# Kernel tuning notes

Hardware: AMD Instinct MI355X
Metric: run time of the kernel (lower is better)

## Reference

```python
import jax, jax.numpy as jnp
import numpy as np

HEADS = 16
EPS = 1e-5

def _ln(x, g, b):
    m = jnp.mean(x, axis=-1, keepdims=True)
    v = jnp.mean((x - m) ** 2, axis=-1, keepdims=True)
    return (x - m) * jax.lax.rsqrt(v + EPS) * g + b

def setup_inputs() -> dict:
    key = jax.random.key(0)
    ks = jax.random.split(key, 12)
    B, N, C, H = 4, 2048, 1024, 4096
    d = {}
    d['x'] = jax.random.normal(ks[0], (B, N, C), jnp.float32)
    d['pos_embed'] = jax.random.normal(ks[1], (1, N, C), jnp.float32)
    # LayerNorm params (normq, normk, normv, norm)
    for nm in ['nq', 'nk', 'nv', 'n']:
        d[nm + '_g'] = jnp.ones((C,), jnp.float32)
        d[nm + '_b'] = jnp.zeros((C,), jnp.float32)
    s = 1.0 / np.sqrt(C)
    d['wq'] = jax.random.uniform(ks[2], (C, C), jnp.float32, -s, s)
    d['bq'] = jnp.zeros((C,), jnp.float32)
    d['wk'] = jax.random.uniform(ks[3], (C, C), jnp.float32, -s, s)
    d['bk'] = jnp.zeros((C,), jnp.float32)
    d['wv'] = jax.random.uniform(ks[4], (C, C), jnp.float32, -s, s)
    d['bv'] = jnp.zeros((C,), jnp.float32)
    d['wp'] = jax.random.uniform(ks[5], (C, C), jnp.float32, -s, s)
    d['bp'] = jnp.zeros((C,), jnp.float32)
    d['w1'] = jax.random.uniform(ks[6], (C, H), jnp.float32, -s, s)
    d['b1'] = jnp.zeros((H,), jnp.float32)
    sh = 1.0 / np.sqrt(H)
    d['w2'] = jax.random.uniform(ks[7], (H, C), jnp.float32, -sh, sh)
    d['b2'] = jnp.zeros((C,), jnp.float32)
    return d

def reference(x, pos_embed, nq_g, nq_b, nk_g, nk_b, nv_g, nv_b, wq, bq, wk, bk, wv, bv, wp, bp, n_g, n_b, w1, b1, w2, b2):
    B, N, C = x.shape
    hd = C // HEADS
    scale = hd ** -0.5
    q_in = x
    k_in = x + pos_embed
    v_in = x + pos_embed
    # Attention (eval mode: dropout = identity)
    q = (_ln(q_in, nq_g, nq_b) @ wq + bq).reshape(B, N, HEADS, hd)
    k = (_ln(k_in, nk_g, nk_b) @ wk + bk).reshape(B, N, HEADS, hd)
    v = (_ln(v_in, nv_g, nv_b) @ wv + bv).reshape(B, N, HEADS, hd)
    attn = jnp.einsum('bqhd,bkhd->bhqk', q, k) * scale
    attn = jax.nn.softmax(attn, axis=-1)
    out = jnp.einsum('bhqk,bkhd->bqhd', attn, v).reshape(B, N, C)
    out = out @ wp + bp
    # residual + MLP
    h = q_in + out
    y = _ln(h, n_g, n_b) @ w1 + b1
    y = jnp.where(y >= 0, y, 0.1 * y)  # LeakyReLU(0.1)
    y = y @ w2 + b2
    return h + y
```

## Files before the change

kernel.cpp:

```cpp
#include <hip/hip_runtime.h>
#include <hip/hip_bf16.h>

#define DEV __device__ __forceinline__

typedef __attribute__((ext_vector_type(8))) short short8;
typedef __attribute__((ext_vector_type(4))) float f32x4;
typedef __attribute__((ext_vector_type(4))) int i32x4;

constexpr int Bb   = 4;
constexpr int SEQ  = 2048;
constexpr int C    = 1024;
constexpr int HID  = 4096;
constexpr int NH   = 16;
constexpr int HD   = 64;
constexpr int MTOT = Bb * SEQ;

DEV unsigned bfbits(float f) {
  unsigned x = __float_as_uint(f);
  return (x + 0x7fffu + ((x >> 16) & 1u)) >> 16;
}

DEV short f2bf(float f) { return (short)bfbits(f); }

DEV unsigned packbf(float a, float b) {
  return bfbits(a) | (bfbits(b) << 16);
}

DEV void gload16(const void* g, void* l) {
  __builtin_amdgcn_global_load_lds((const __attribute__((address_space(1))) void*)g,
                                   (__attribute__((address_space(3))) void*)l, 16, 0, 0);
}

__global__ void k_transpose_w(const float* __restrict__ src, short* __restrict__ dst,
                              int R, int Cc) {
  __shared__ float t[32][33];
  int tx = threadIdx.x & 31, ty = threadIdx.x >> 5;
  int c0 = blockIdx.x * 32, r0 = blockIdx.y * 32;
  #pragma unroll
  for (int i = 0; i < 4; i++)
    t[ty + i * 8][tx] = src[(size_t)(r0 + ty + i * 8) * Cc + c0 + tx];
  __syncthreads();
  #pragma unroll
  for (int i = 0; i < 4; i++)
    dst[(size_t)(c0 + ty + i * 8) * R + r0 + tx] = f2bf(t[tx][ty + i * 8]);
}

__global__ void k_transpose_v(const short* __restrict__ V, short* __restrict__ Vt) {
  __shared__ short t[32][33];
  int tx = threadIdx.x & 31, ty = threadIdx.x >> 5;
  int plane = blockIdx.z;
  int b = plane >> 4, h = plane & 15;
  int n0 = blockIdx.x * 32, d0 = blockIdx.y * 32;
  #pragma unroll
  for (int i = 0; i < 4; i++)
    t[ty + i * 8][tx] = V[(size_t)(b * SEQ + n0 + ty + i * 8) * C + h * HD + d0 + tx];
  __syncthreads();
  #pragma unroll
  for (int i = 0; i < 4; i++)
    Vt[((size_t)plane * HD + d0 + ty + i * 8) * SEQ + n0 + tx] = t[tx][ty + i * 8];
}

__global__ void k_ln_qkv(const float* __restrict__ x, const float* __restrict__ pos,
                         const float* __restrict__ nqg, const float* __restrict__ nqb,
                         const float* __restrict__ nkg, const float* __restrict__ nkb,
                         const float* __restrict__ nvg, const float* __restrict__ nvb,
                         short* __restrict__ xq, short* __restrict__ xk,
                         short* __restrict__ xv) {
  int row = blockIdx.x, tid = threadIdx.x;
  int n = row & (SEQ - 1);
  float a4[4], p4[4];
  float s1 = 0, s2 = 0, t1 = 0, t2 = 0;
  #pragma unroll
  for (int i = 0; i < 4; i++) {
    int c = tid + i * 256;
    float a = x[(size_t)row * C + c];
    float p = pos[(size_t)n * C + c] + a;
    a4[i] = a; p4[i] = p;
    s1 += a; s2 += a * a; t1 += p; t2 += p * p;
  }
  #pragma unroll
  for (int off = 32; off; off >>= 1) {
    s1 += __shfl_xor(s1, off, 64);
    s2 += __shfl_xor(s2, off, 64);
    t1 += __shfl_xor(t1, off, 64);
    t2 += __shfl_xor(t2, off, 64);
  }
  __shared__ float red[4][4];
  int wave = tid >> 6, lane = tid & 63;
  if (lane == 0) { red[wave][0] = s1; red[wave][1] = s2; red[wave][2] = t1; red[wave][3] = t2; }
  __syncthreads();
  s1 = red[0][0] + red[1][0] + red[2][0] + red[3][0];
  s2 = red[0][1] + red[1][1] + red[2][1] + red[3][1];
  t1 = red[0][2] + red[1][2] + red[2][2] + red[3][2];
  t2 = red[0][3] + red[1][3] + red[2][3] + red[3][3];
  float mq = s1 * (1.f / C), mk = t1 * (1.f / C);
  float rq = rsqrtf(s2 * (1.f / C) - mq * mq + 1e-5f);
  float rk = rsqrtf(t2 * (1.f / C) - mk * mk + 1e-5f);
  #pragma unroll
  for (int i = 0; i < 4; i++) {
    int c = tid + i * 256;
    float nq_ = (a4[i] - mq) * rq;
    float nk_ = (p4[i] - mk) * rk;
    xq[(size_t)row * C + c] = f2bf(nq_ * nqg[c] + nqb[c]);
    xk[(size_t)row * C + c] = f2bf(nk_ * nkg[c] + nkb[c]);
    xv[(size_t)row * C + c] = f2bf(nk_ * nvg[c] + nvb[c]);
  }
}

__global__ void k_ln1(const float* __restrict__ h, const float* __restrict__ g,
                      const float* __restrict__ bta, short* __restrict__ out) {
  int row = blockIdx.x, tid = threadIdx.x;
  float a4[4];
  float s1 = 0, s2 = 0;
  #pragma unroll
  for (int i = 0; i < 4; i++) {
    int c = tid + i * 256;
    float a = h[(size_t)row * C + c];
    a4[i] = a; s1 += a; s2 += a * a;
  }
  #pragma unroll
  for (int off = 32; off; off >>= 1) {
    s1 += __shfl_xor(s1, off, 64);
    s2 += __shfl_xor(s2, off, 64);
  }
  __shared__ float red[4][2];
  int wave = tid >> 6, lane = tid & 63;
  if (lane == 0) { red[wave][0] = s1; red[wave][1] = s2; }
  __syncthreads();
  s1 = red[0][0] + red[1][0] + red[2][0] + red[3][0];
  s2 = red[0][1] + red[1][1] + red[2][1] + red[3][1];
  float m = s1 * (1.f / C);
  float r = rsqrtf(s2 * (1.f / C) - m * m + 1e-5f);
  #pragma unroll
  for (int i = 0; i < 4; i++) {
    int c = tid + i * 256;
    out[(size_t)row * C + c] = f2bf((a4[i] - m) * r * g[c] + bta[c]);
  }
}

template <int MODE>
__global__ __launch_bounds__(256, 2)
void k_gemm(const short* __restrict__ A, const short* __restrict__ Bt,
            const float* __restrict__ bias, const float* __restrict__ resid,
            void* __restrict__ outp, int Nn, int Kk) {
  __shared__ short sA[128 * 32];
  __shared__ short sB[128 * 32];
  const int tid = threadIdx.x;
  const int n0 = blockIdx.x * 128, m0 = blockIdx.y * 128;
  const int wave = tid >> 6, lane = tid & 63, quad = lane >> 4, l15 = lane & 15;
  const int wm = (wave >> 1) * 64, wn = (wave & 1) * 64;

  const int r0 = tid >> 2, s0 = (tid & 3) * 8;
  const short* gA0 = A + (size_t)(m0 + r0) * Kk + s0;
  const short* gA1 = A + (size_t)(m0 + r0 + 64) * Kk + s0;
  const short* gB0 = Bt + (size_t)(n0 + r0) * Kk + s0;
  const short* gB1 = Bt + (size_t)(n0 + r0 + 64) * Kk + s0;
  short* lA0 = &sA[tid * 8];
  short* lA1 = &sA[(tid + 256) * 8];
  short* lB0 = &sB[tid * 8];
  short* lB1 = &sB[(tid + 256) * 8];

  const f32x4 fzero = {0.f, 0.f, 0.f, 0.f};
  f32x4 acc[4][4];
  #pragma unroll
  for (int mi = 0; mi < 4; mi++)
    #pragma unroll
    for (int ni = 0; ni < 4; ni++) acc[mi][ni] = fzero;

  for (int k0 = 0; k0 < Kk; k0 += 32) {
    gload16(gA0 + k0, lA0);
    gload16(gA1 + k0, lA1);
    gload16(gB0 + k0, lB0);
    gload16(gB1 + k0, lB1);
    __syncthreads();
    short8 av[4], bv[4];
    #pragma unroll
    for (int mi = 0; mi < 4; mi++)
      av[mi] = *(const short8*)&sA[(wm + mi * 16 + l15) * 32 + quad * 8];
    #pragma unroll
    for (int ni = 0; ni < 4; ni++)
      bv[ni] = *(const short8*)&sB[(wn + ni * 16 + l15) * 32 + quad * 8];
    #pragma unroll
    for (int mi = 0; mi < 4; mi++)
      #pragma unroll
      for (int ni = 0; ni < 4; ni++)
        acc[mi][ni] = __builtin_amdgcn_mfma_f32_16x16x32_bf16(av[mi], bv[ni], acc[mi][ni], 0, 0, 0);
    __syncthreads();
  }

  float bb[4];
  #pragma unroll
  for (int ni = 0; ni < 4; ni++) bb[ni] = bias[n0 + wn + ni * 16 + l15];

  #pragma unroll
  for (int mi = 0; mi < 4; mi++) {
    #pragma unroll
    for (int ni = 0; ni < 4; ni++) {
      #pragma unroll
      for (int r = 0; r < 4; r++) {
        int row = m0 + wm + mi * 16 + quad * 4 + r;
        int col = n0 + wn + ni * 16 + l15;
        float v = acc[mi][ni][r] + bb[ni];
        if constexpr (MODE == 1) v = v >= 0.f ? v : 0.1f * v;
        if constexpr (MODE == 3) v *= 0.125f;
        if constexpr (MODE == 2)
          ((float*)outp)[(size_t)row * Nn + col] = resid[(size_t)row * Nn + col] + v;
        else
          ((short*)outp)[(size_t)row * Nn + col] = f2bf(v);
      }
    }
  }
}

__global__ __launch_bounds__(256, 4)
void k_attn(const short* __restrict__ Q, const short* __restrict__ K,
            const short* __restrict__ Vt, short* __restrict__ O) {
  constexpr int LD = 72;
  __shared__ short sQ[128 * LD];
  __shared__ short sK[64 * LD];
  __shared__ short sV[64 * LD];
  const int tid = threadIdx.x;
  const int bh = blockIdx.y;
  const int b = bh >> 4, h = bh & 15;
  const int q0 = blockIdx.x * 128;
  const int wave = tid >> 6, lane = tid & 63, quad = lane >> 4, l15 = lane & 15;
  const int wm = wave * 32;
  const size_t tokBase = (size_t)b * SEQ;

  #pragma unroll
  for (int i = 0; i < 4; i++) {
    int idx = tid + i * 256, row = idx >> 3, seg = idx & 7;
    *(int4*)&sQ[row * LD + seg * 8] =
        *(const int4*)(Q + (tokBase + q0 + row) * C + h * HD + seg * 8);
  }

  const f32x4 fzero = {0.f, 0.f, 0.f, 0.f};
  f32x4 o[2][4];
  float lsum[2] = {0.f, 0.f};
  #pragma unroll
  for (int qi = 0; qi < 2; qi++)
    #pragma unroll
    for (int di = 0; di < 4; di++) o[qi][di] = fzero;

  const int selHi = quad >> 1;
  const int srcL0 = ((quad & 1) * 2) * 16 + l15;
  const int srcL1 = ((quad & 1) * 2 + 1) * 16 + l15;

  for (int kb = 0; kb < SEQ / 64; kb++) {
    const int k0 = kb * 64;
    __syncthreads();
    #pragma unroll
    for (int i = 0; i < 2; i++) {
      int idx = tid + i * 256, row = idx >> 3, seg = idx & 7;
      *(int4*)&sK[row * LD + seg * 8] =
          *(const int4*)(K + (tokBase + k0 + row) * C + h * HD + seg * 8);
      *(int4*)&sV[row * LD + seg * 8] =
          *(const int4*)(Vt + ((size_t)bh * HD + row) * SEQ + k0 + seg * 8);
    }
    __syncthreads();

    unsigned pk[4][2][2];
    float csum[2] = {0.f, 0.f};
    #pragma unroll
    for (int qi = 0; qi < 2; qi++) {
      short8 b0 = *(const short8*)&sQ[(wm + qi * 16 + l15) * LD + quad * 8];
      short8 b1 = *(const short8*)&sQ[(wm + qi * 16 + l15) * LD + 32 + quad * 8];
      #pragma unroll
      for (int ki = 0; ki < 4; ki++) {
        short8 a0 = *(const short8*)&sK[(ki * 16 + l15) * LD + quad * 8];
        short8 a1 = *(const short8*)&sK[(ki * 16 + l15) * LD + 32 + quad * 8];
        f32x4 st = __builtin_amdgcn_mfma_f32_16x16x32_bf16(a0, b0, fzero, 0, 0, 0);
        st = __builtin_amdgcn_mfma_f32_16x16x32_bf16(a1, b1, st, 0, 0, 0);
        float p0 = __expf(st[0]), p1 = __expf(st[1]);
        float p2 = __expf(st[2]), p3 = __expf(st[3]);
        csum[qi] += (p0 + p1) + (p2 + p3);
        pk[ki][qi][0] = packbf(p0, p1);
        pk[ki][qi][1] = packbf(p2, p3);
      }
    }
    #pragma unroll
    for (int qi = 0; qi < 2; qi++) {
      float v = csum[qi];
      v += __shfl_xor(v, 16, 64);
      v += __shfl_xor(v, 32, 64);
      lsum[qi] += v;
    }

    #pragma unroll
    for (int kc = 0; kc < 2; kc++) {
      #pragma unroll
      for (int qi = 0; qi < 2; qi++) {
        i32x4 fr;
        int vA, vB;
        vA = __shfl((int)pk[2 * kc][qi][0], srcL0, 64);
        vB = __shfl((int)pk[2 * kc + 1][qi][0], srcL0, 64);
        fr.x = selHi ? vB : vA;
        vA = __shfl((int)pk[2 * kc][qi][1], srcL0, 64);
        vB = __shfl((int)pk[2 * kc + 1][qi][1], srcL0, 64);
        fr.y = selHi ? vB : vA;
        vA = __shfl((int)pk[2 * kc][qi][0], srcL1, 64);
        vB = __shfl((int)pk[2 * kc + 1][qi][0], srcL1, 64);
        fr.z = selHi ? vB : vA;
        vA = __shfl((int)pk[2 * kc][qi][1], srcL1, 64);
        vB = __shfl((int)pk[2 * kc + 1][qi][1], srcL1, 64);
        fr.w = selHi ? vB : vA;
        short8 aP = __builtin_bit_cast(short8, fr);
        #pragma unroll
        for (int di = 0; di < 4; di++) {
          short8 bv = *(const short8*)&sV[(di * 16 + l15) * LD + kc * 32 + quad * 8];
          o[qi][di] = __builtin_amdgcn_mfma_f32_16x16x32_bf16(aP, bv, o[qi][di], 0, 0, 0);
        }
      }
    }
  }

  float linv[2][4];
  #pragma unroll
  for (int qi = 0; qi < 2; qi++)
    #pragma unroll
    for (int r = 0; r < 4; r++)
      linv[qi][r] = 1.0f / __shfl(lsum[qi], quad * 4 + r, 64);

  #pragma unroll
  for (int qi = 0; qi < 2; qi++)
    #pragma unroll
    for (int di = 0; di < 4; di++)
      #pragma unroll
      for (int r = 0; r < 4; r++) {
        int row = q0 + wm + qi * 16 + quad * 4 + r;
        int col = h * HD + di * 16 + l15;
        O[(tokBase + row) * C + col] = f2bf(o[qi][di][r] * linv[qi][r]);
      }
}

extern "C" void kernel_launch(void* const* d_in, const int* in_sizes, int n_in,
                              void* d_out, int out_size, void* d_ws, size_t ws_size,
                              hipStream_t stream) {
  const float* x   = (const float*)d_in[0];
  const float* pos = (const float*)d_in[1];
  const float* nqg = (const float*)d_in[2];
  const float* nqb = (const float*)d_in[3];
  const float* nkg = (const float*)d_in[4];
  const float* nkb = (const float*)d_in[5];
  const float* nvg = (const float*)d_in[6];
  const float* nvb = (const float*)d_in[7];
  const float* ng  = (const float*)d_in[8];
  const float* nb  = (const float*)d_in[9];
  const float* wq  = (const float*)d_in[10];
  const float* bq  = (const float*)d_in[11];
  const float* wk  = (const float*)d_in[12];
  const float* bk  = (const float*)d_in[13];
  const float* wv  = (const float*)d_in[14];
  const float* bv  = (const float*)d_in[15];
  const float* wp  = (const float*)d_in[16];
  const float* bp  = (const float*)d_in[17];
  const float* w1  = (const float*)d_in[18];
  const float* b1  = (const float*)d_in[19];
  const float* w2  = (const float*)d_in[20];
  const float* b2  = (const float*)d_in[21];

  char* ws = (char*)d_ws;
  const size_t MB = 1u << 20;
  short* wqT  = (short*)(ws + 0 * MB);
  short* wkT  = (short*)(ws + 2 * MB);
  short* wvT  = (short*)(ws + 4 * MB);
  short* wpT  = (short*)(ws + 6 * MB);
  short* w1T  = (short*)(ws + 8 * MB);
  short* w2T  = (short*)(ws + 16 * MB);
  short* xq   = (short*)(ws + 24 * MB);
  short* xk   = (short*)(ws + 40 * MB);
  short* xv   = (short*)(ws + 56 * MB);
  short* Qm   = (short*)(ws + 72 * MB);
  short* Km   = (short*)(ws + 88 * MB);
  short* Vm   = (short*)(ws + 104 * MB);
  short* Vt   = (short*)(ws + 120 * MB);
  short* y1   = (short*)(ws + 72 * MB);
  short* Ob   = xk;
  short* hln  = xq;
  float* hbuf = (float*)(ws + 136 * MB);
  (void)ws_size; (void)in_sizes; (void)n_in; (void)out_size;

  dim3 blk(256);
  k_transpose_w<<<dim3(32, 32),  blk, 0, stream>>>(wq, wqT, C, C);
  k_transpose_w<<<dim3(32, 32),  blk, 0, stream>>>(wk, wkT, C, C);
  k_transpose_w<<<dim3(32, 32),  blk, 0, stream>>>(wv, wvT, C, C);
  k_transpose_w<<<dim3(32, 32),  blk, 0, stream>>>(wp, wpT, C, C);
  k_transpose_w<<<dim3(128, 32), blk, 0, stream>>>(w1, w1T, C, HID);
  k_transpose_w<<<dim3(32, 128), blk, 0, stream>>>(w2, w2T, HID, C);
  k_ln_qkv<<<dim3(MTOT), blk, 0, stream>>>(x, pos, nqg, nqb, nkg, nkb, nvg, nvb, xq, xk, xv);
  k_gemm<3><<<dim3(C / 128, MTOT / 128), blk, 0, stream>>>(xq, wqT, bq, nullptr, Qm, C, C);
  k_gemm<0><<<dim3(C / 128, MTOT / 128), blk, 0, stream>>>(xk, wkT, bk, nullptr, Km, C, C);
  k_gemm<0><<<dim3(C / 128, MTOT / 128), blk, 0, stream>>>(xv, wvT, bv, nullptr, Vm, C, C);
  k_transpose_v<<<dim3(SEQ / 32, HD / 32, Bb * NH), blk, 0, stream>>>(Vm, Vt);
  k_attn<<<dim3(SEQ / 128, Bb * NH), blk, 0, stream>>>(Qm, Km, Vt, Ob);
  k_gemm<2><<<dim3(C / 128, MTOT / 128), blk, 0, stream>>>(Ob, wpT, bp, x, hbuf, C, C);
  k_ln1<<<dim3(MTOT), blk, 0, stream>>>(hbuf, ng, nb, hln);
  k_gemm<1><<<dim3(HID / 128, MTOT / 128), blk, 0, stream>>>(hln, w1T, b1, nullptr, y1, HID, C);
  k_gemm<2><<<dim3(C / 128, MTOT / 128), blk, 0, stream>>>(y1, w2T, b2, hbuf, (float*)d_out, C, HID);
}
```

Measured before the change: 627.7 us.

## Double-buffer attention K/V tiles with async LDS loads and register-resident Q

The attention kernel now double-buffers the K and V tiles through direct global-to-LDS loads, so the next tile is fetched while the current one is computed, and it drops one barrier per iteration. Q fragments stay in registers, K/V use an XOR-swizzled LDS layout without padding, and V fragments are loaded once per kc. The Q scale folds in log2(e) so the kernel can use exp2f, and bf16 packing uses a cheaper round-half-up perm. The grid is transposed so that blocks of the same head run together. The costs are less precise bf16 rounding and reliance on a single barrier per iteration for buffer reuse.

After: 619.2 us. About the same (-1.4%).

```diff
diff --git a/kernel.cpp b/kernel.cpp
--- a/kernel.cpp
+++ b/kernel.cpp
@@ -22,8 +22,10 @@
 
 DEV short f2bf(float f) { return (short)bfbits(f); }
 
-DEV unsigned packbf(float a, float b) {
-  return bfbits(a) | (bfbits(b) << 16);
+DEV unsigned packrn(float a, float b) {
+  unsigned ua = __float_as_uint(a) + 0x8000u;
+  unsigned ub = __float_as_uint(b) + 0x8000u;
+  return __builtin_amdgcn_perm(ub, ua, 0x07060302u);
 }
 
 DEV void gload16(const void* g, void* l) {
@@ -202,7 +204,7 @@
         int col = n0 + wn + ni * 16 + l15;
         float v = acc[mi][ni][r] + bb[ni];
         if constexpr (MODE == 1) v = v >= 0.f ? v : 0.1f * v;
-        if constexpr (MODE == 3) v *= 0.125f;
+        if constexpr (MODE == 3) v *= 0.1803368801111244f;
         if constexpr (MODE == 2)
           ((float*)outp)[(size_t)row * Nn + col] = resid[(size_t)row * Nn + col] + v;
         else
@@ -215,24 +217,42 @@
 __global__ __launch_bounds__(256, 4)
 void k_attn(const short* __restrict__ Q, const short* __restrict__ K,
             const short* __restrict__ Vt, short* __restrict__ O) {
-  constexpr int LD = 72;
-  __shared__ short sQ[128 * LD];
-  __shared__ short sK[64 * LD];
-  __shared__ short sV[64 * LD];
+  __shared__ __align__(16) short sK[2][64 * 64];
+  __shared__ __align__(16) short sV[2][64 * 64];
   const int tid = threadIdx.x;
-  const int bh = blockIdx.y;
+  const int bh = blockIdx.x;
   const int b = bh >> 4, h = bh & 15;
-  const int q0 = blockIdx.x * 128;
+  const int q0 = blockIdx.y * 128;
   const int wave = tid >> 6, lane = tid & 63, quad = lane >> 4, l15 = lane & 15;
   const int wm = wave * 32;
   const size_t tokBase = (size_t)b * SEQ;
 
-  #pragma unroll
-  for (int i = 0; i < 4; i++) {
-    int idx = tid + i * 256, row = idx >> 3, seg = idx & 7;
-    *(int4*)&sQ[row * LD + seg * 8] =
-        *(const int4*)(Q + (tokBase + q0 + row) * C + h * HD + seg * 8);
-  }
+  short8 qf[2][2];
+  #pragma unroll
+  for (int qi = 0; qi < 2; qi++)
+    #pragma unroll
+    for (int hf = 0; hf < 2; hf++)
+      qf[qi][hf] = *(const short8*)(Q + (tokBase + q0 + wm + qi * 16 + l15) * C
+                                    + h * HD + hf * 32 + quad * 8);
+
+  const int r0 = tid >> 3,        c0s = ((tid & 7) ^ (r0 & 7)) * 8;
+  const int r1 = (tid + 256) >> 3, c1s = ((tid & 7) ^ (r1 & 7)) * 8;
+  const short* gK0 = K + (tokBase + r0) * C + h * HD + c0s;
+  const short* gK1 = K + (tokBase + r1) * C + h * HD + c1s;
+  const short* gV0 = Vt + ((size_t)bh * HD + r0) * SEQ + c0s;
+  const short* gV1 = Vt + ((size_t)bh * HD + r1) * SEQ + c1s;
+  short* lK0 = &sK[0][tid * 8];
+  short* lK1 = &sK[0][(tid + 256) * 8];
+  short* lV0 = &sV[0][tid * 8];
+  short* lV1 = &sV[0][(tid + 256) * 8];
+  constexpr int BUFO = 64 * 64;
+
+#define STAGE(bufsel, kb) {                                   \
+    int kk = (kb) * 64, bo = (bufsel) * BUFO;                 \
+    gload16(gK0 + (size_t)kk * C, lK0 + bo);                  \
+    gload16(gK1 + (size_t)kk * C, lK1 + bo);                  \
+    gload16(gV0 + kk,             lV0 + bo);                  \
+    gload16(gV1 + kk,             lV1 + bo); }
 
   const f32x4 fzero = {0.f, 0.f, 0.f, 0.f};
   f32x4 o[2][4];
@@ -245,37 +265,31 @@
   const int selHi = quad >> 1;
   const int srcL0 = ((quad & 1) * 2) * 16 + l15;
   const int srcL1 = ((quad & 1) * 2 + 1) * 16 + l15;
+  const int sw = l15 & 7;
+
+  STAGE(0, 0)
 
   for (int kb = 0; kb < SEQ / 64; kb++) {
-    const int k0 = kb * 64;
+    const int buf = kb & 1;
     __syncthreads();
-    #pragma unroll
-    for (int i = 0; i < 2; i++) {
-      int idx = tid + i * 256, row = idx >> 3, seg = idx & 7;
-      *(int4*)&sK[row * LD + seg * 8] =
-          *(const int4*)(K + (tokBase + k0 + row) * C + h * HD + seg * 8);
-      *(int4*)&sV[row * LD + seg * 8] =
-          *(const int4*)(Vt + ((size_t)bh * HD + row) * SEQ + k0 + seg * 8);
-    }
-    __syncthreads();
+    if (kb + 1 < SEQ / 64) STAGE(buf ^ 1, kb + 1)
 
     unsigned pk[4][2][2];
     float csum[2] = {0.f, 0.f};
     #pragma unroll
-    for (int qi = 0; qi < 2; qi++) {
-      short8 b0 = *(const short8*)&sQ[(wm + qi * 16 + l15) * LD + quad * 8];
-      short8 b1 = *(const short8*)&sQ[(wm + qi * 16 + l15) * LD + 32 + quad * 8];
-      #pragma unroll
-      for (int ki = 0; ki < 4; ki++) {
-        short8 a0 = *(const short8*)&sK[(ki * 16 + l15) * LD + quad * 8];
-        short8 a1 = *(const short8*)&sK[(ki * 16 + l15) * LD + 32 + quad * 8];
-        f32x4 st = __builtin_amdgcn_mfma_f32_16x16x32_bf16(a0, b0, fzero, 0, 0, 0);
-        st = __builtin_amdgcn_mfma_f32_16x16x32_bf16(a1, b1, st, 0, 0, 0);
-        float p0 = __expf(st[0]), p1 = __expf(st[1]);
-        float p2 = __expf(st[2]), p3 = __expf(st[3]);
+    for (int ki = 0; ki < 4; ki++) {
+      const int krow = (ki * 16 + l15) * 64;
+      short8 a0 = *(const short8*)&sK[buf][krow + ((0 + quad) ^ sw) * 8];
+      short8 a1 = *(const short8*)&sK[buf][krow + ((4 + quad) ^ sw) * 8];
+      #pragma unroll
+      for (int qi = 0; qi < 2; qi++) {
+        f32x4 st = __builtin_amdgcn_mfma_f32_16x16x32_bf16(a0, qf[qi][0], fzero, 0, 0, 0);
+        st = __builtin_amdgcn_mfma_f32_16x16x32_bf16(a1, qf[qi][1], st, 0, 0, 0);
+        float p0 = exp2f(st[0]), p1 = exp2f(st[1]);
+        float p2 = exp2f(st[2]), p3 = exp2f(st[3]);
         csum[qi] += (p0 + p1) + (p2 + p3);
-        pk[ki][qi][0] = packbf(p0, p1);
-        pk[ki][qi][1] = packbf(p2, p3);
+        pk[ki][qi][0] = packrn(p0, p1);
+        pk[ki][qi][1] = packrn(p2, p3);
       }
     }
     #pragma unroll
@@ -288,6 +302,10 @@
 
     #pragma unroll
     for (int kc = 0; kc < 2; kc++) {
+      short8 bv[4];
+      #pragma unroll
+      for (int di = 0; di < 4; di++)
+        bv[di] = *(const short8*)&sV[buf][(di * 16 + l15) * 64 + ((kc * 4 + quad) ^ sw) * 8];
       #pragma unroll
       for (int qi = 0; qi < 2; qi++) {
         i32x4 fr;
@@ -306,13 +324,12 @@
         fr.w = selHi ? vB : vA;
         short8 aP = __builtin_bit_cast(short8, fr);
         #pragma unroll
-        for (int di = 0; di < 4; di++) {
-          short8 bv = *(const short8*)&sV[(di * 16 + l15) * LD + kc * 32 + quad * 8];
-          o[qi][di] = __builtin_amdgcn_mfma_f32_16x16x32_bf16(aP, bv, o[qi][di], 0, 0, 0);
-        }
+        for (int di = 0; di < 4; di++)
+          o[qi][di] = __builtin_amdgcn_mfma_f32_16x16x32_bf16(aP, bv[di], o[qi][di], 0, 0, 0);
       }
     }
   }
+#undef STAGE
 
   float linv[2][4];
   #pragma unroll
@@ -392,7 +409,7 @@
   k_gemm<0><<<dim3(C / 128, MTOT / 128), blk, 0, stream>>>(xk, wkT, bk, nullptr, Km, C, C);
   k_gemm<0><<<dim3(C / 128, MTOT / 128), blk, 0, stream>>>(xv, wvT, bv, nullptr, Vm, C, C);
   k_transpose_v<<<dim3(SEQ / 32, HD / 32, Bb * NH), blk, 0, stream>>>(Vm, Vt);
-  k_attn<<<dim3(SEQ / 128, Bb * NH), blk, 0, stream>>>(Qm, Km, Vt, Ob);
+  k_attn<<<dim3(Bb * NH, SEQ / 128), blk, 0, stream>>>(Qm, Km, Vt, Ob);
   k_gemm<2><<<dim3(C / 128, MTOT / 128), blk, 0, stream>>>(Ob, wpT, bp, x, hbuf, C, C);
   k_ln1<<<dim3(MTOT), blk, 0, stream>>>(hbuf, ng, nb, hln);
   k_gemm<1><<<dim3(HID / 128, MTOT / 128), blk, 0, stream>>>(hln, w1T, b1, nullptr, y1, HID, C);
```
